# Kernel tuning notes

Measured on AMD Instinct MI355X. Metric: run time of the kernel, lower is better.

## Reference

```python
import jax, jax.numpy as jnp
import numpy as np

B, S, D, H, O, E, TOPK = 4, 2048, 512, 1024, 512, 8, 2


def setup_inputs() -> dict:
    key = jax.random.key(0)
    ks = jax.random.split(key, 6)
    s = lambda d: 1.0 / np.sqrt(d)
    return {
        "x": jax.random.normal(ks[0], (B, S, D), dtype=jnp.float32),
        "Wg": jax.random.normal(ks[1], (D, E), dtype=jnp.float32) * s(D),
        "W1": jax.random.normal(ks[2], (E, D, H), dtype=jnp.float32) * s(D),
        "b1": jnp.zeros((E, H), dtype=jnp.float32),
        "W2": jax.random.normal(ks[3], (E, H, O), dtype=jnp.float32) * s(H),
        "b2": jnp.zeros((E, O), dtype=jnp.float32),
    }


def reference(x, Wg, W1, b1, W2, b2):
    Bsz, Seq, Din = x.shape
    T = Bsz * Seq
    xm = x.reshape(T, Din)                       # [T, D] token matrix
    # router: softmax over experts, then top-k (ProbabilitySamplerTopk)
    probs = jax.nn.softmax(xm @ Wg, axis=-1)     # [T, E]
    top_p, top_i = jax.lax.top_k(probs, TOPK)    # [T, k]
    # dense scattered gates (topKProbabilitiesScattered in _computeGating);
    # zero entries for non-selected experts make the einsum combine exactly
    # equal to the original gather->per-expert-GEMM->index_add pipeline.
    gates = jnp.zeros((T, E), dtype=probs.dtype).at[
        jnp.arange(T)[:, None], top_i
    ].set(top_p)                                 # [T, E]
    # per-expert 2-layer MLP (inputExperts -> activation -> outputExperts)
    h = jax.nn.gelu(jnp.einsum("td,edh->teh", xm, W1) + b1[None])  # [T, E, H]
    y = jnp.einsum("teh,eho->teo", h, W2) + b2[None]               # [T, E, O]
    # weighted combine (multiply_by_gates + index_add)
    out = jnp.einsum("te,teo->to", gates, y)     # [T, O]
    return out.reshape(Bsz, Seq, O)
```

## Files before the change

### kernel.cpp

```cpp
#include <hip/hip_runtime.h>

#define T_TOK 8192
#define DIM   512
#define HID   1024
#define OUTD  512
#define NE    8

typedef __attribute__((ext_vector_type(8))) short short8v;
typedef __attribute__((ext_vector_type(4))) float f32x4;

__device__ __forceinline__ unsigned short f2bf(float f) {
  unsigned int u = __builtin_bit_cast(unsigned int, f);
  u += 0x7fffu + ((u >> 16) & 1u);
  return (unsigned short)(u >> 16);
}

__device__ __forceinline__ float bf2f(unsigned short h) {
  unsigned int u = ((unsigned int)h) << 16;
  return __builtin_bit_cast(float, u);
}

__device__ __forceinline__ void gload_lds16(const void* g, void* l) {
  __builtin_amdgcn_global_load_lds(
      (__attribute__((address_space(1))) void*)g,
      (__attribute__((address_space(3))) void*)l, 16, 0, 0);
}

__device__ __forceinline__ float gelu_f(float v) {
  const float c0 = 0.7978845608028654f;
  float u = c0 * (v + 0.044715f * v * v * v);
  return v / (1.0f + __expf(-2.0f * u));
}

__global__ __launch_bounds__(256) void k_prep(
    const float* __restrict__ W1, const float* __restrict__ W2,
    unsigned short* __restrict__ W1t, unsigned short* __restrict__ W2t,
    const float* __restrict__ x, const float* __restrict__ Wg,
    int* __restrict__ top_e, float* __restrict__ top_p) {
  int bid = blockIdx.x;
  int tid = threadIdx.x;
  if (bid < 8192) {
    __shared__ float tile[32][33];
    int which = bid >> 12;
    int r = bid & 4095;
    int e = r >> 9;
    int t = r & 511;
    int R = which ? HID : DIM;
    int C = which ? OUTD : HID;
    int tx, ty;
    if (which == 0) { ty = t >> 5; tx = t & 31; }
    else            { ty = t >> 4; tx = t & 15; }
    const float* inE = (which ? W2 : W1) + (size_t)e * R * C;
    unsigned short* outE = (which ? W2t : W1t) + (size_t)e * R * C;
    int c0 = tx * 32, r0 = ty * 32;
    int xx = tid & 31, yy = tid >> 5;
#pragma unroll
    for (int i = 0; i < 32; i += 8)
      tile[yy + i][xx] = inE[(size_t)(r0 + yy + i) * C + (c0 + xx)];
    __syncthreads();
#pragma unroll
    for (int i = 0; i < 32; i += 8)
      outE[(size_t)(c0 + yy + i) * R + (r0 + xx)] = f2bf(tile[xx][yy + i]);
  } else {
    int lane = tid & 63;
    int t = (bid - 8192) * 4 + (tid >> 6);
    const float* xr = x + (size_t)t * DIM;
    int j0 = lane * 8;
    float4 xa = *(const float4*)(xr + j0);
    float4 xb = *(const float4*)(xr + j0 + 4);
    float xl[8] = {xa.x, xa.y, xa.z, xa.w, xb.x, xb.y, xb.z, xb.w};
    float acc[8] = {0.f,0.f,0.f,0.f,0.f,0.f,0.f,0.f};
#pragma unroll
    for (int jj = 0; jj < 8; ++jj) {
      float4 w0 = *(const float4*)(Wg + (size_t)(j0 + jj) * NE);
      float4 w1 = *(const float4*)(Wg + (size_t)(j0 + jj) * NE + 4);
      acc[0] += xl[jj] * w0.x; acc[1] += xl[jj] * w0.y;
      acc[2] += xl[jj] * w0.z; acc[3] += xl[jj] * w0.w;
      acc[4] += xl[jj] * w1.x; acc[5] += xl[jj] * w1.y;
      acc[6] += xl[jj] * w1.z; acc[7] += xl[jj] * w1.w;
    }
#pragma unroll
    for (int off = 32; off >= 1; off >>= 1) {
#pragma unroll
      for (int e2 = 0; e2 < 8; ++e2) acc[e2] += __shfl_xor(acc[e2], off, 64);
    }
    if (lane == 0) {
      float m = acc[0];
#pragma unroll
      for (int e2 = 1; e2 < 8; ++e2) m = fmaxf(m, acc[e2]);
      float p[8]; float s = 0.f;
#pragma unroll
      for (int e2 = 0; e2 < 8; ++e2) { p[e2] = expf(acc[e2] - m); s += p[e2]; }
      float inv = 1.f / s;
      int i0 = 0;
#pragma unroll
      for (int e2 = 1; e2 < 8; ++e2) if (p[e2] > p[i0]) i0 = e2;
      int i1 = (i0 == 0) ? 1 : 0;
#pragma unroll
      for (int e2 = 0; e2 < 8; ++e2) if (e2 != i0 && p[e2] > p[i1]) i1 = e2;
      top_e[t * 2] = i0;  top_e[t * 2 + 1] = i1;
      top_p[t * 2] = p[i0] * inv;  top_p[t * 2 + 1] = p[i1] * inv;
    }
  }
}

__global__ __launch_bounds__(256) void k_plan(
    const int* __restrict__ top_e, int* __restrict__ localRank,
    int* __restrict__ blockCounts) {
  __shared__ int cnt[4][NE];
  __shared__ int wbase[4][NE];
  int tid = threadIdx.x, lane = tid & 63, w = tid >> 6;
  int a = blockIdx.x * 256 + tid;
  int e = top_e[a];
  int rank = 0;
#pragma unroll
  for (int e2 = 0; e2 < NE; ++e2) {
    unsigned long long m = __ballot(e == e2);
    if (e == e2) rank = __popcll(m & ((1ULL << lane) - 1ULL));
    if (lane == 0) cnt[w][e2] = __popcll(m);
  }
  __syncthreads();
  if (tid < NE) {
    int s = 0;
#pragma unroll
    for (int w2 = 0; w2 < 4; ++w2) { wbase[w2][tid] = s; s += cnt[w2][tid]; }
    blockCounts[blockIdx.x * NE + tid] = s;
  }
  __syncthreads();
  localRank[a] = wbase[w][e] + rank;
}

__global__ __launch_bounds__(256) void k_scatter(
    const float* __restrict__ x, const int* __restrict__ top_e,
    const int* __restrict__ localRank, const int* __restrict__ blockCounts,
    int* __restrict__ offs, int* __restrict__ pos_of,
    unsigned short* __restrict__ Xp) {
  __shared__ int sBase[NE];
  __shared__ int sTot[NE];
  __shared__ int sOffs[NE];
  int tid = threadIdx.x;
  int g = blockIdx.x >> 6;
  if (tid < NE) {
    int pre = 0, tot = 0;
    for (int b = 0; b < 64; ++b) {
      int c = blockCounts[b * NE + tid];
      if (b < g) pre += c;
      tot += c;
    }
    sBase[tid] = pre; sTot[tid] = tot;
  }
  __syncthreads();
  if (tid == 0) {
    int s = 0;
#pragma unroll
    for (int e = 0; e < NE; ++e) { sOffs[e] = s; s += sTot[e]; }
    if (blockIdx.x == 0) {
      for (int e = 0; e < NE; ++e) offs[e] = sOffs[e];
      offs[NE] = s;
    }
  }
  __syncthreads();
  int lane = tid & 63;
  int a = blockIdx.x * 4 + (tid >> 6);
  int t = a >> 1;
  int e = top_e[a];
  int pos = sOffs[e] + sBase[e] + localRank[a];
  if (lane == 0) pos_of[a] = pos;
  const float* xr = x + (size_t)t * DIM + lane * 8;
  float4 xa = *(const float4*)xr;
  float4 xb = *(const float4*)(xr + 4);
  short8v pk;
  pk[0] = (short)f2bf(xa.x); pk[1] = (short)f2bf(xa.y);
  pk[2] = (short)f2bf(xa.z); pk[3] = (short)f2bf(xa.w);
  pk[4] = (short)f2bf(xb.x); pk[5] = (short)f2bf(xb.y);
  pk[6] = (short)f2bf(xb.z); pk[7] = (short)f2bf(xb.w);
  *(short8v*)(Xp + (size_t)pos * DIM + lane * 8) = pk;
}

#define MFMA1(d, a, b) d = __builtin_amdgcn_mfma_f32_16x16x32_bf16(a, b, d, 0, 0, 0)

template<int NX, int LOG2NX>
__global__ __launch_bounds__(512, 4) void k_gemm_w(
    const unsigned short* __restrict__ A, const unsigned short* __restrict__ Bt,
    const float* __restrict__ bias, const int* __restrict__ offs,
    unsigned short* __restrict__ Hout, int K, int N) {
  __shared__ __align__(16) unsigned short Al[256 * 64];
  __shared__ __align__(16) unsigned short Bl[128 * 64];

  const int e = blockIdx.x & 7;
  const int slot = blockIdx.x >> 3;
  const int nSlots = gridDim.x >> 3;
  const int rowBeg = offs[e], rowEnd = offs[e + 1];
  if (rowBeg >= rowEnd) return;
  const int nMT = (rowEnd - rowBeg + 255) >> 8;
  const int nWork = nMT << LOG2NX;
  const unsigned short* Be = Bt + (size_t)e * N * K;

  const int tid = threadIdx.x, lane = tid & 63, w = tid >> 6;
  const int wm = w >> 1, wn = w & 1;
  const int fr = lane & 15, fq = lane >> 4;
  const int sRow = tid >> 3;
  const int sCe = ((((tid & 7) << 4) ^ ((sRow & 7) << 4)) >> 1);
  const int NT = K >> 6;

  for (int idx = slot; idx < nWork; idx += nSlots) {
    const int mt = idx >> LOG2NX;
    const int xb = idx & (NX - 1);
    const int m0 = rowBeg + mt * 256;
    const int n0 = xb * 128;

    const char* aP[4]; const char* bP[2];
#pragma unroll
    for (int c_ = 0; c_ < 4; ++c_) {
      int ar_ = m0 + c_ * 64 + sRow; if (ar_ > rowEnd - 1) ar_ = rowEnd - 1;
      aP[c_] = (const char*)(A + (size_t)ar_ * K + sCe);
    }
#pragma unroll
    for (int c_ = 0; c_ < 2; ++c_) {
      int br_ = n0 + c_ * 64 + sRow;
      bP[c_] = (const char*)(Be + (size_t)br_ * K + sCe);
    }

    f32x4 acc[4][4];
#pragma unroll
    for (int m = 0; m < 4; ++m)
#pragma unroll
      for (int n = 0; n < 4; ++n) acc[m][n] = (f32x4){0.f, 0.f, 0.f, 0.f};

    for (int t = 0; t < NT; ++t) {
      const int tOff = t << 7;
#pragma unroll
      for (int c_ = 0; c_ < 4; ++c_)
        gload_lds16(aP[c_] + tOff, (char*)&Al[0] + c_ * 8192 + (w << 10));
#pragma unroll
      for (int c_ = 0; c_ < 2; ++c_)
        gload_lds16(bP[c_] + tOff, (char*)&Bl[0] + c_ * 8192 + (w << 10));
      __syncthreads();
#pragma unroll
      for (int kk = 0; kk < 2; ++kk) {
        short8v av[4], bv[4];
#pragma unroll
        for (int m = 0; m < 4; ++m) {
          int row_ = wm * 64 + m * 16 + fr;
          av[m] = *(const short8v*)((const char*)&Al[0] + row_ * 128 +
                    (((kk << 6) + (fq << 4)) ^ ((fr & 7) << 4)));
        }
#pragma unroll
        for (int n = 0; n < 4; ++n) {
          int row_ = wn * 64 + n * 16 + fr;
          bv[n] = *(const short8v*)((const char*)&Bl[0] + row_ * 128 +
                    (((kk << 6) + (fq << 4)) ^ ((fr & 7) << 4)));
        }
#pragma unroll
        for (int m = 0; m < 4; ++m)
#pragma unroll
          for (int n = 0; n < 4; ++n)
            MFMA1(acc[m][n], av[m], bv[n]);
      }
      __syncthreads();
    }

#pragma unroll
    for (int m = 0; m < 4; ++m) {
#pragma unroll
      for (int j = 0; j < 4; ++j) {
        int row = m0 + wm * 64 + m * 16 + fq * 4 + j;
        if (row >= rowEnd) continue;
#pragma unroll
        for (int n = 0; n < 4; ++n) {
          int col = n0 + wn * 64 + n * 16 + fr;
          float v = acc[m][n][j] + bias[(size_t)e * N + col];
          Hout[(size_t)row * N + col] = f2bf(gelu_f(v));
        }
      }
    }
  }
}

template<int NX, int LOG2NX>
__global__ __launch_bounds__(256, 2) void k_gemm_y(
    const unsigned short* __restrict__ A,
    const unsigned short* __restrict__ Bt,
    const float* __restrict__ bias, const int* __restrict__ offs,
    unsigned short* __restrict__ Ybf, int K, int N) {
  __shared__ __align__(16) unsigned short Al[128 * 128];
  __shared__ __align__(16) unsigned short Bl[128 * 128];

  const int e = blockIdx.x & 7;
  const int slot = blockIdx.x >> 3;
  const int nSlots = gridDim.x >> 3;
  const int rowBeg = offs[e], rowEnd = offs[e + 1];
  if (rowBeg >= rowEnd) return;
  const int nMT = (rowEnd - rowBeg + 127) >> 7;
  const int nWork = nMT << LOG2NX;
  const unsigned short* Be = Bt + (size_t)e * N * K;

  const int tid = threadIdx.x, lane = tid & 63, w = tid >> 6;
  const int wr = w >> 1, wc = w & 1;
  const int fr = lane & 15, fq = lane >> 4;
  const int sRow = tid >> 4;
  const int sCb = (((tid & 15) << 4) ^ ((sRow & 7) << 4));
  const int NT = K >> 7;

  for (int idx = slot; idx < nWork; idx += nSlots) {
    const int mt = idx >> LOG2NX;
    const int xb = idx & (NX - 1);
    const int m0 = rowBeg + mt * 128;
    const int n0 = xb * 128;

    const char* aP[8];
#pragma unroll
    for (int c_ = 0; c_ < 8; ++c_) {
      int ar_ = m0 + c_ * 16 + sRow; if (ar_ > rowEnd - 1) ar_ = rowEnd - 1;
      aP[c_] = (const char*)(A + (size_t)ar_ * K) + sCb;
    }
    const char* bP0 = (const char*)(Be + (size_t)(n0 + sRow) * K) + sCb;
    const int bStride = 16 * K * 2;

    f32x4 acc[4][4];
#pragma unroll
    for (int m = 0; m < 4; ++m)
#pragma unroll
      for (int n = 0; n < 4; ++n) acc[m][n] = (f32x4){0.f, 0.f, 0.f, 0.f};

    for (int t = 0; t < NT; ++t) {
      const int tOff = t << 8;
#pragma unroll
      for (int c_ = 0; c_ < 8; ++c_)
        gload_lds16(aP[c_] + tOff, (char*)&Al[0] + c_ * 4096 + (tid << 4));
#pragma unroll
      for (int c_ = 0; c_ < 8; ++c_)
        gload_lds16(bP0 + c_ * bStride + tOff, (char*)&Bl[0] + c_ * 4096 + (tid << 4));
      __syncthreads();
#pragma unroll
      for (int kk = 0; kk < 4; ++kk) {
        short8v av[4], bv[4];
#pragma unroll
        for (int m = 0; m < 4; ++m) {
          int row_ = wr * 64 + m * 16 + fr;
          av[m] = *(const short8v*)((const char*)&Al[0] + row_ * 256 +
                    (((kk << 6) + (fq << 4)) ^ ((fr & 7) << 4)));
        }
#pragma unroll
        for (int n = 0; n < 4; ++n) {
          int row_ = wc * 64 + n * 16 + fr;
          bv[n] = *(const short8v*)((const char*)&Bl[0] + row_ * 256 +
                    (((kk << 6) + (fq << 4)) ^ ((fr & 7) << 4)));
        }
#pragma unroll
        for (int m = 0; m < 4; ++m)
#pragma unroll
          for (int n = 0; n < 4; ++n)
            MFMA1(acc[m][n], av[m], bv[n]);
      }
      __syncthreads();
    }

#pragma unroll
    for (int m = 0; m < 4; ++m) {
#pragma unroll
      for (int j = 0; j < 4; ++j) {
        int row = m0 + wr * 64 + m * 16 + fq * 4 + j;
        if (row >= rowEnd) continue;
#pragma unroll
        for (int n = 0; n < 4; ++n) {
          int col = n0 + wc * 64 + n * 16 + fr;
          float v = acc[m][n][j] + bias[(size_t)e * N + col];
          Ybf[(size_t)row * N + col] = f2bf(v);
        }
      }
    }
  }
}

__global__ __launch_bounds__(256) void k_combine(
    const unsigned short* __restrict__ Y, const int* __restrict__ pos_of,
    const float* __restrict__ top_p, float* __restrict__ out) {
  int lane = threadIdx.x & 63;
  int t = blockIdx.x * 4 + (threadIdx.x >> 6);
  int p0 = pos_of[t * 2], p1 = pos_of[t * 2 + 1];
  float g0 = top_p[t * 2], g1 = top_p[t * 2 + 1];
  short8v ya = *(const short8v*)(Y + (size_t)p0 * OUTD + lane * 8);
  short8v yb = *(const short8v*)(Y + (size_t)p1 * OUTD + lane * 8);
  float4 r0, r1;
  r0.x = g0 * bf2f((unsigned short)ya[0]) + g1 * bf2f((unsigned short)yb[0]);
  r0.y = g0 * bf2f((unsigned short)ya[1]) + g1 * bf2f((unsigned short)yb[1]);
  r0.z = g0 * bf2f((unsigned short)ya[2]) + g1 * bf2f((unsigned short)yb[2]);
  r0.w = g0 * bf2f((unsigned short)ya[3]) + g1 * bf2f((unsigned short)yb[3]);
  r1.x = g0 * bf2f((unsigned short)ya[4]) + g1 * bf2f((unsigned short)yb[4]);
  r1.y = g0 * bf2f((unsigned short)ya[5]) + g1 * bf2f((unsigned short)yb[5]);
  r1.z = g0 * bf2f((unsigned short)ya[6]) + g1 * bf2f((unsigned short)yb[6]);
  r1.w = g0 * bf2f((unsigned short)ya[7]) + g1 * bf2f((unsigned short)yb[7]);
  float4* o = (float4*)(out + (size_t)t * OUTD + lane * 8);
  o[0] = r0; o[1] = r1;
}

extern "C" void kernel_launch(void* const* d_in, const int* in_sizes, int n_in,
                              void* d_out, int out_size, void* d_ws, size_t ws_size,
                              hipStream_t stream) {
  const float* x  = (const float*)d_in[0];
  const float* Wg = (const float*)d_in[1];
  const float* W1 = (const float*)d_in[2];
  const float* b1 = (const float*)d_in[3];
  const float* W2 = (const float*)d_in[4];
  const float* b2 = (const float*)d_in[5];
  float* out = (float*)d_out;

  char* p = (char*)d_ws;
  auto take = [&](size_t bytes) { char* r = p; p += (bytes + 255) & ~(size_t)255; return r; };
  unsigned short* W1t = (unsigned short*)take((size_t)NE * DIM * HID * 2);
  unsigned short* W2t = (unsigned short*)take((size_t)NE * HID * OUTD * 2);
  unsigned short* Xp  = (unsigned short*)take((size_t)2 * T_TOK * DIM * 2);
  unsigned short* Hb  = (unsigned short*)take((size_t)2 * T_TOK * HID * 2);
  unsigned short* Yb  = (unsigned short*)take((size_t)2 * T_TOK * OUTD * 2);
  int* offs   = (int*)take(4096);
  int*   top_e  = (int*)take((size_t)2 * T_TOK * 4);
  float* top_pv = (float*)take((size_t)2 * T_TOK * 4);
  int*   pos_of = (int*)take((size_t)2 * T_TOK * 4);
  int* localRank   = (int*)take((size_t)2 * T_TOK * 4);
  int* blockCounts = (int*)take((size_t)64 * NE * 4);

  const int PLAN_BLOCKS = (2 * T_TOK) / 256;

  k_prep<<<8192 + 2048, 256, 0, stream>>>(W1, W2, W1t, W2t, x, Wg, top_e, top_pv);
  k_plan<<<PLAN_BLOCKS, 256, 0, stream>>>(top_e, localRank, blockCounts);
  k_scatter<<<(2 * T_TOK) / 4, 256, 0, stream>>>(x, top_e, localRank, blockCounts,
                                                 offs, pos_of, Xp);
  k_gemm_w<8, 3><<<1024, 512, 0, stream>>>(Xp, W1t, b1, offs, Hb, DIM, HID);
  k_gemm_y<4, 2><<<512, 256, 0, stream>>>(Hb, W2t, b2, offs, Yb, HID, OUTD);
  k_combine<<<T_TOK / 4, 256, 0, stream>>>(Yb, pos_of, top_pv, out);
}
```

Before: 126.9 us.

## Regroup prep kernels: separate router, merge scatter with weight transpose

Splits the router out of the prep kernel and launches it alone first. The bf16 weight transpose now shares a launch with the token scatter, so the router-to-plan critical path no longer waits on the large weight conversion. The first GEMM's grid is also halved from 1024 to 512 blocks. The regrouping keeps the launch count the same while moving the transpose work off the path the routing stages depend on. The smaller GEMM grid may change load balance across CUs.

```diff
diff --git a/kernel.cpp b/kernel.cpp
--- a/kernel.cpp
+++ b/kernel.cpp
@@ -32,17 +32,130 @@
   return v / (1.0f + __expf(-2.0f * u));
 }
 
-__global__ __launch_bounds__(256) void k_prep(
-    const float* __restrict__ W1, const float* __restrict__ W2,
-    unsigned short* __restrict__ W1t, unsigned short* __restrict__ W2t,
+__global__ __launch_bounds__(256) void k_router(
     const float* __restrict__ x, const float* __restrict__ Wg,
     int* __restrict__ top_e, float* __restrict__ top_p) {
+  int lane = threadIdx.x & 63;
+  int t = blockIdx.x * 4 + (threadIdx.x >> 6);
+  const float* xr = x + (size_t)t * DIM;
+  int j0 = lane * 8;
+  float4 xa = *(const float4*)(xr + j0);
+  float4 xb = *(const float4*)(xr + j0 + 4);
+  float xl[8] = {xa.x, xa.y, xa.z, xa.w, xb.x, xb.y, xb.z, xb.w};
+  float acc[8] = {0.f,0.f,0.f,0.f,0.f,0.f,0.f,0.f};
+#pragma unroll
+  for (int jj = 0; jj < 8; ++jj) {
+    float4 w0 = *(const float4*)(Wg + (size_t)(j0 + jj) * NE);
+    float4 w1 = *(const float4*)(Wg + (size_t)(j0 + jj) * NE + 4);
+    acc[0] += xl[jj] * w0.x; acc[1] += xl[jj] * w0.y;
+    acc[2] += xl[jj] * w0.z; acc[3] += xl[jj] * w0.w;
+    acc[4] += xl[jj] * w1.x; acc[5] += xl[jj] * w1.y;
+    acc[6] += xl[jj] * w1.z; acc[7] += xl[jj] * w1.w;
+  }
+#pragma unroll
+  for (int off = 32; off >= 1; off >>= 1) {
+#pragma unroll
+    for (int e2 = 0; e2 < 8; ++e2) acc[e2] += __shfl_xor(acc[e2], off, 64);
+  }
+  if (lane == 0) {
+    float m = acc[0];
+#pragma unroll
+    for (int e2 = 1; e2 < 8; ++e2) m = fmaxf(m, acc[e2]);
+    float p[8]; float s = 0.f;
+#pragma unroll
+    for (int e2 = 0; e2 < 8; ++e2) { p[e2] = expf(acc[e2] - m); s += p[e2]; }
+    float inv = 1.f / s;
+    int i0 = 0;
+#pragma unroll
+    for (int e2 = 1; e2 < 8; ++e2) if (p[e2] > p[i0]) i0 = e2;
+    int i1 = (i0 == 0) ? 1 : 0;
+#pragma unroll
+    for (int e2 = 0; e2 < 8; ++e2) if (e2 != i0 && p[e2] > p[i1]) i1 = e2;
+    top_e[t * 2] = i0;  top_e[t * 2 + 1] = i1;
+    top_p[t * 2] = p[i0] * inv;  top_p[t * 2 + 1] = p[i1] * inv;
+  }
+}
+
+__global__ __launch_bounds__(256) void k_plan(
+    const int* __restrict__ top_e, int* __restrict__ localRank,
+    int* __restrict__ blockCounts) {
+  __shared__ int cnt[4][NE];
+  __shared__ int wbase[4][NE];
+  int tid = threadIdx.x, lane = tid & 63, w = tid >> 6;
+  int a = blockIdx.x * 256 + tid;
+  int e = top_e[a];
+  int rank = 0;
+#pragma unroll
+  for (int e2 = 0; e2 < NE; ++e2) {
+    unsigned long long m = __ballot(e == e2);
+    if (e == e2) rank = __popcll(m & ((1ULL << lane) - 1ULL));
+    if (lane == 0) cnt[w][e2] = __popcll(m);
+  }
+  __syncthreads();
+  if (tid < NE) {
+    int s = 0;
+#pragma unroll
+    for (int w2 = 0; w2 < 4; ++w2) { wbase[w2][tid] = s; s += cnt[w2][tid]; }
+    blockCounts[blockIdx.x * NE + tid] = s;
+  }
+  __syncthreads();
+  localRank[a] = wbase[w][e] + rank;
+}
+
+__global__ __launch_bounds__(256) void k_work(
+    const float* __restrict__ x, const int* __restrict__ top_e,
+    const int* __restrict__ localRank, const int* __restrict__ blockCounts,
+    int* __restrict__ offs, int* __restrict__ pos_of,
+    unsigned short* __restrict__ Xp,
+    const float* __restrict__ W1, const float* __restrict__ W2,
+    unsigned short* __restrict__ W1t, unsigned short* __restrict__ W2t) {
   int bid = blockIdx.x;
   int tid = threadIdx.x;
-  if (bid < 8192) {
+  if (bid < 4096) {
+    __shared__ int sBase[NE];
+    __shared__ int sTot[NE];
+    __shared__ int sOffs[NE];
+    int g = bid >> 6;
+    if (tid < NE) {
+      int pre = 0, tot = 0;
+      for (int b = 0; b < 64; ++b) {
+        int c = blockCounts[b * NE + tid];
+        if (b < g) pre += c;
+        tot += c;
+      }
+      sBase[tid] = pre; sTot[tid] = tot;
+    }
+    __syncthreads();
+    if (tid == 0) {
+      int s = 0;
+#pragma unroll
+      for (int e = 0; e < NE; ++e) { sOffs[e] = s; s += sTot[e]; }
+      if (bid == 0) {
+        for (int e = 0; e < NE; ++e) offs[e] = sOffs[e];
+        offs[NE] = s;
+      }
+    }
+    __syncthreads();
+    int lane = tid & 63;
+    int a = bid * 4 + (tid >> 6);
+    int t = a >> 1;
+    int e = top_e[a];
+    int pos = sOffs[e] + sBase[e] + localRank[a];
+    if (lane == 0) pos_of[a] = pos;
+    const float* xr = x + (size_t)t * DIM + lane * 8;
+    float4 xa = *(const float4*)xr;
+    float4 xb = *(const float4*)(xr + 4);
+    short8v pk;
+    pk[0] = (short)f2bf(xa.x); pk[1] = (short)f2bf(xa.y);
+    pk[2] = (short)f2bf(xa.z); pk[3] = (short)f2bf(xa.w);
+    pk[4] = (short)f2bf(xb.x); pk[5] = (short)f2bf(xb.y);
+    pk[6] = (short)f2bf(xb.z); pk[7] = (short)f2bf(xb.w);
+    *(short8v*)(Xp + (size_t)pos * DIM + lane * 8) = pk;
+  } else {
     __shared__ float tile[32][33];
-    int which = bid >> 12;
-    int r = bid & 4095;
+    int b2 = bid - 4096;
+    int which = b2 >> 12;
+    int r = b2 & 4095;
     int e = r >> 9;
     int t = r & 511;
     int R = which ? HID : DIM;
@@ -61,120 +174,7 @@
 #pragma unroll
     for (int i = 0; i < 32; i += 8)
       outE[(size_t)(c0 + yy + i) * R + (r0 + xx)] = f2bf(tile[xx][yy + i]);
-  } else {
-    int lane = tid & 63;
-    int t = (bid - 8192) * 4 + (tid >> 6);
-    const float* xr = x + (size_t)t * DIM;
-    int j0 = lane * 8;
-    float4 xa = *(const float4*)(xr + j0);
-    float4 xb = *(const float4*)(xr + j0 + 4);
-    float xl[8] = {xa.x, xa.y, xa.z, xa.w, xb.x, xb.y, xb.z, xb.w};
-    float acc[8] = {0.f,0.f,0.f,0.f,0.f,0.f,0.f,0.f};
-#pragma unroll
-    for (int jj = 0; jj < 8; ++jj) {
-      float4 w0 = *(const float4*)(Wg + (size_t)(j0 + jj) * NE);
-      float4 w1 = *(const float4*)(Wg + (size_t)(j0 + jj) * NE + 4);
-      acc[0] += xl[jj] * w0.x; acc[1] += xl[jj] * w0.y;
-      acc[2] += xl[jj] * w0.z; acc[3] += xl[jj] * w0.w;
-      acc[4] += xl[jj] * w1.x; acc[5] += xl[jj] * w1.y;
-      acc[6] += xl[jj] * w1.z; acc[7] += xl[jj] * w1.w;
-    }
-#pragma unroll
-    for (int off = 32; off >= 1; off >>= 1) {
-#pragma unroll
-      for (int e2 = 0; e2 < 8; ++e2) acc[e2] += __shfl_xor(acc[e2], off, 64);
-    }
-    if (lane == 0) {
-      float m = acc[0];
-#pragma unroll
-      for (int e2 = 1; e2 < 8; ++e2) m = fmaxf(m, acc[e2]);
-      float p[8]; float s = 0.f;
-#pragma unroll
-      for (int e2 = 0; e2 < 8; ++e2) { p[e2] = expf(acc[e2] - m); s += p[e2]; }
-      float inv = 1.f / s;
-      int i0 = 0;
-#pragma unroll
-      for (int e2 = 1; e2 < 8; ++e2) if (p[e2] > p[i0]) i0 = e2;
-      int i1 = (i0 == 0) ? 1 : 0;
-#pragma unroll
-      for (int e2 = 0; e2 < 8; ++e2) if (e2 != i0 && p[e2] > p[i1]) i1 = e2;
-      top_e[t * 2] = i0;  top_e[t * 2 + 1] = i1;
-      top_p[t * 2] = p[i0] * inv;  top_p[t * 2 + 1] = p[i1] * inv;
-    }
-  }
-}
-
-__global__ __launch_bounds__(256) void k_plan(
-    const int* __restrict__ top_e, int* __restrict__ localRank,
-    int* __restrict__ blockCounts) {
-  __shared__ int cnt[4][NE];
-  __shared__ int wbase[4][NE];
-  int tid = threadIdx.x, lane = tid & 63, w = tid >> 6;
-  int a = blockIdx.x * 256 + tid;
-  int e = top_e[a];
-  int rank = 0;
-#pragma unroll
-  for (int e2 = 0; e2 < NE; ++e2) {
-    unsigned long long m = __ballot(e == e2);
-    if (e == e2) rank = __popcll(m & ((1ULL << lane) - 1ULL));
-    if (lane == 0) cnt[w][e2] = __popcll(m);
-  }
-  __syncthreads();
-  if (tid < NE) {
-    int s = 0;
-#pragma unroll
-    for (int w2 = 0; w2 < 4; ++w2) { wbase[w2][tid] = s; s += cnt[w2][tid]; }
-    blockCounts[blockIdx.x * NE + tid] = s;
-  }
-  __syncthreads();
-  localRank[a] = wbase[w][e] + rank;
-}
-
-__global__ __launch_bounds__(256) void k_scatter(
-    const float* __restrict__ x, const int* __restrict__ top_e,
-    const int* __restrict__ localRank, const int* __restrict__ blockCounts,
-    int* __restrict__ offs, int* __restrict__ pos_of,
-    unsigned short* __restrict__ Xp) {
-  __shared__ int sBase[NE];
-  __shared__ int sTot[NE];
-  __shared__ int sOffs[NE];
-  int tid = threadIdx.x;
-  int g = blockIdx.x >> 6;
-  if (tid < NE) {
-    int pre = 0, tot = 0;
-    for (int b = 0; b < 64; ++b) {
-      int c = blockCounts[b * NE + tid];
-      if (b < g) pre += c;
-      tot += c;
-    }
-    sBase[tid] = pre; sTot[tid] = tot;
-  }
-  __syncthreads();
-  if (tid == 0) {
-    int s = 0;
-#pragma unroll
-    for (int e = 0; e < NE; ++e) { sOffs[e] = s; s += sTot[e]; }
-    if (blockIdx.x == 0) {
-      for (int e = 0; e < NE; ++e) offs[e] = sOffs[e];
-      offs[NE] = s;
-    }
-  }
-  __syncthreads();
-  int lane = tid & 63;
-  int a = blockIdx.x * 4 + (tid >> 6);
-  int t = a >> 1;
-  int e = top_e[a];
-  int pos = sOffs[e] + sBase[e] + localRank[a];
-  if (lane == 0) pos_of[a] = pos;
-  const float* xr = x + (size_t)t * DIM + lane * 8;
-  float4 xa = *(const float4*)xr;
-  float4 xb = *(const float4*)(xr + 4);
-  short8v pk;
-  pk[0] = (short)f2bf(xa.x); pk[1] = (short)f2bf(xa.y);
-  pk[2] = (short)f2bf(xa.z); pk[3] = (short)f2bf(xa.w);
-  pk[4] = (short)f2bf(xb.x); pk[5] = (short)f2bf(xb.y);
-  pk[6] = (short)f2bf(xb.z); pk[7] = (short)f2bf(xb.w);
-  *(short8v*)(Xp + (size_t)pos * DIM + lane * 8) = pk;
+  }
 }
 
 #define MFMA1(d, a, b) d = __builtin_amdgcn_mfma_f32_16x16x32_bf16(a, b, d, 0, 0, 0)
@@ -422,11 +422,11 @@
 
   const int PLAN_BLOCKS = (2 * T_TOK) / 256;
 
-  k_prep<<<8192 + 2048, 256, 0, stream>>>(W1, W2, W1t, W2t, x, Wg, top_e, top_pv);
+  k_router<<<T_TOK / 4, 256, 0, stream>>>(x, Wg, top_e, top_pv);
   k_plan<<<PLAN_BLOCKS, 256, 0, stream>>>(top_e, localRank, blockCounts);
-  k_scatter<<<(2 * T_TOK) / 4, 256, 0, stream>>>(x, top_e, localRank, blockCounts,
-                                                 offs, pos_of, Xp);
-  k_gemm_w<8, 3><<<1024, 512, 0, stream>>>(Xp, W1t, b1, offs, Hb, DIM, HID);
+  k_work<<<4096 + 8192, 256, 0, stream>>>(x, top_e, localRank, blockCounts,
+                                          offs, pos_of, Xp, W1, W2, W1t, W2t);
+  k_gemm_w<8, 3><<<512, 512, 0, stream>>>(Xp, W1t, b1, offs, Hb, DIM, HID);
   k_gemm_y<4, 2><<<512, 256, 0, stream>>>(Hb, W2t, b2, offs, Yb, HID, OUTD);
   k_combine<<<T_TOK / 4, 256, 0, stream>>>(Yb, pos_of, top_pv, out);
 }
```

Result: no change. 126.8 us (-0.1%).
